# Performance work log

Measured on AMD Instinct MI355X. Metric: run time of the kernel, lower is better.

## Reference

```python
import jax, jax.numpy as jnp
import numpy as np

NUM_HEADS = 8
HEAD_DIM = 128
ATTN_SCALE = 0.12


def _rotary_tables(T, head_dim, dtype=jnp.float32):
    # modded-nanogpt half-truncated RoPE: rotate only first half of freq slots
    quarter = head_dim // 4
    angular = (1.0 / 1024.0) ** jnp.linspace(0.0, 1.0, quarter, dtype=dtype)
    angular = jnp.concatenate([angular, jnp.zeros(quarter, dtype=dtype)])  # [head_dim//2]
    t = jnp.arange(T, dtype=dtype)
    theta = t[:, None] * angular[None, :]  # [T, head_dim//2]
    return jnp.cos(theta), jnp.sin(theta)


def _apply_rotary(x, cos, sin):
    # x: [B, T, H, D]; cos/sin: [T, D//2]
    x1, x2 = jnp.split(x, 2, axis=-1)
    c = cos[None, :, None, :]
    s = sin[None, :, None, :]
    y1 = x1 * c + x2 * s
    y2 = -x1 * s + x2 * c
    return jnp.concatenate([y1, y2], axis=-1)


def _rms_norm(x):
    eps = jnp.asarray(jnp.finfo(x.dtype).eps, x.dtype)
    var = jnp.mean(jnp.square(x), axis=-1, keepdims=True)
    return x * jax.lax.rsqrt(var + eps)


def setup_inputs() -> dict:
    key = jax.random.key(0)
    k1, k2, k3, k4, k5 = jax.random.split(key, 5)
    B, T, D = 1, 4096, 1024
    hdim = NUM_HEADS * HEAD_DIM
    std = 0.5 * D ** (-0.5)
    x = jax.random.normal(k1, (B, T, D), dtype=jnp.float32)
    ve = jax.random.normal(k2, (B, T, hdim), dtype=jnp.float32)
    qkv_w = jax.random.normal(k3, (3, hdim, D), dtype=jnp.float32) * std
    lambdas = jnp.array([0.5, 0.5], dtype=jnp.float32)
    c_proj_w = jax.random.normal(k5, (D, hdim), dtype=jnp.float32) * std
    return {"x": x, "ve": ve, "qkv_w": qkv_w, "lambdas": lambdas, "c_proj_w": c_proj_w}


def reference(x, ve, qkv_w, lambdas, c_proj_w):
    B, T, D = x.shape
    H, Hd = NUM_HEADS, HEAD_DIM
    # QKV projection: qkv_w [3, H*Hd, D]
    qkv = jnp.einsum('btd,ckd->btck', x, qkv_w)  # [B, T, 3, H*Hd]
    qkv = qkv.reshape(B, T, 3, H, Hd)
    q, k, v = qkv[:, :, 0], qkv[:, :, 1], qkv[:, :, 2]  # [B, T, H, Hd]
    # QK RMSNorm
    q = _rms_norm(q)
    k = _rms_norm(k)
    # RoPE
    cos, sin = _rotary_tables(T, Hd, dtype=x.dtype)
    q = _apply_rotary(q, cos, sin)
    k = _apply_rotary(k, cos, sin)
    # value-embedding lambda mix
    v = lambdas[0] * v + lambdas[1] * ve.reshape(B, T, H, Hd)
    # causal attention with fixed scale 0.12 (block-causal FlexAttention mask)
    scores = jnp.einsum('bthd,bshd->bhts', q, k) * ATTN_SCALE  # [B, H, T, T]
    causal = jnp.tril(jnp.ones((T, T), dtype=bool))
    scores = jnp.where(causal[None, None], scores, jnp.asarray(-jnp.inf, scores.dtype))
    probs = jax.nn.softmax(scores, axis=-1)
    y = jnp.einsum('bhts,bshd->bthd', probs, v)  # [B, T, H, Hd]
    y = y.reshape(B, T, H * Hd)
    return y @ c_proj_w.T  # [B, T, D]
```

## Files before the change

### kernel.cpp

```cpp
#include <hip/hip_runtime.h>

typedef __bf16 bf16;
typedef __bf16 bf16x8 __attribute__((ext_vector_type(8)));
typedef __bf16 bf16x4 __attribute__((ext_vector_type(4)));
typedef __bf16 bf16x2 __attribute__((ext_vector_type(2)));
typedef float f32x4 __attribute__((ext_vector_type(4)));
typedef float f32x16 __attribute__((ext_vector_type(16)));
typedef int i32x4 __attribute__((ext_vector_type(4)));

#define GLL16(gp, lp)                                                          \
  __builtin_amdgcn_global_load_lds(                                            \
      (const __attribute__((address_space(1))) unsigned int*)(gp),             \
      (__attribute__((address_space(3))) unsigned int*)(lp), 16, 0, 0)

__global__ __launch_bounds__(256) void cast3_f32_bf16(
    const float* __restrict__ a, bf16* __restrict__ oa, int na4,
    const float* __restrict__ b, bf16* __restrict__ ob, int nb4,
    const float* __restrict__ c, bf16* __restrict__ oc, int nc4) {
  int i = blockIdx.x * blockDim.x + threadIdx.x;
  int stride = gridDim.x * blockDim.x;
  int total = na4 + nb4 + nc4;
  for (; i < total; i += stride) {
    const float4* src;
    bf16x4* dst;
    int j = i;
    if (j < na4) {
      src = (const float4*)a + j; dst = (bf16x4*)oa + j;
    } else if ((j -= na4) < nb4) {
      src = (const float4*)b + j; dst = (bf16x4*)ob + j;
    } else {
      j -= nb4;
      src = (const float4*)c + j; dst = (bf16x4*)oc + j;
    }
    float4 v = *src;
    bf16x4 o;
    o[0] = (bf16)v.x; o[1] = (bf16)v.y; o[2] = (bf16)v.z; o[3] = (bf16)v.w;
    *dst = o;
  }
}

template <int K, int LDC, typename CT>
__global__ __launch_bounds__(256) void gemm_bt(
    const bf16* __restrict__ A, const bf16* __restrict__ B,
    CT* __restrict__ C) {
  __shared__ __align__(16) bf16 As[128 * 64];
  __shared__ __align__(16) bf16 Bs[128 * 64];
  const int tid  = threadIdx.x;
  const int lane = tid & 63;
  const int wave = tid >> 6;
  const int ln15 = lane & 15, quad = lane >> 4;
  const int wm = wave >> 1, wn = wave & 1;
  const int m0 = blockIdx.y * 128, n0 = blockIdx.x * 128;

  f32x4 acc[4][4] = {};

  for (int k0 = 0; k0 < K; k0 += 64) {
    __syncthreads();
#pragma unroll
    for (int j = 0; j < 4; ++j) {
      int gbase = j * 256 + wave * 64;
      int g = gbase + lane;
      int r = g >> 3, c = (g & 7) ^ (r & 7);
      GLL16(A + (size_t)(m0 + r) * K + k0 + c * 8, As + (size_t)gbase * 8);
    }
#pragma unroll
    for (int j = 0; j < 4; ++j) {
      int gbase = j * 256 + wave * 64;
      int g = gbase + lane;
      int r = g >> 3, c = (g & 7) ^ (r & 7);
      GLL16(B + (size_t)(n0 + r) * K + k0 + c * 8, Bs + (size_t)gbase * 8);
    }
    __syncthreads();
#pragma unroll
    for (int kk = 0; kk < 2; ++kk) {
      bf16x8 af[4], bfr[4];
#pragma unroll
      for (int mi = 0; mi < 4; ++mi) {
        int m = wm * 64 + mi * 16 + ln15;
        int cg = kk * 4 + quad;
        af[mi] = *(const bf16x8*)(As + (m * 8 + (cg ^ (m & 7))) * 8);
      }
#pragma unroll
      for (int ni = 0; ni < 4; ++ni) {
        int n = wn * 64 + ni * 16 + ln15;
        int cg = kk * 4 + quad;
        bfr[ni] = *(const bf16x8*)(Bs + (n * 8 + (cg ^ (n & 7))) * 8);
      }
#pragma unroll
      for (int mi = 0; mi < 4; ++mi)
#pragma unroll
        for (int ni = 0; ni < 4; ++ni)
          acc[mi][ni] = __builtin_amdgcn_mfma_f32_16x16x32_bf16(
              af[mi], bfr[ni], acc[mi][ni], 0, 0, 0);
    }
  }
#pragma unroll
  for (int mi = 0; mi < 4; ++mi)
#pragma unroll
    for (int ni = 0; ni < 4; ++ni)
#pragma unroll
      for (int r = 0; r < 4; ++r) {
        int row = m0 + wm * 64 + mi * 16 + quad * 4 + r;
        int col = n0 + wn * 64 + ni * 16 + ln15;
        C[(size_t)row * LDC + col] = (CT)acc[mi][ni][r];
      }
}

__global__ __launch_bounds__(256) void qkv_post(
    const bf16* __restrict__ qkv, const float* __restrict__ ve,
    const float* __restrict__ lambdas, bf16* __restrict__ qn,
    bf16* __restrict__ kn, bf16* __restrict__ vt) {
  const int h  = blockIdx.x;
  const int t0 = blockIdx.y * 64;
  const int tid = threadIdx.x;
  const int wave = tid >> 6, lane = tid & 63;
  __shared__ __align__(16) float tile[64][129];

  const int j = lane;
  float cth = 1.0f, sth = 0.0f;
  for (int i = 0; i < 16; ++i) {
    int t = t0 + wave * 16 + i;
    if (j < 32) {
      float ang = exp2f((float)j * (-10.0f / 31.0f));
      float th = (float)t * ang;
      __sincosf(th, &sth, &cth);
    }
#pragma unroll
    for (int qk = 0; qk < 2; ++qk) {
      const bf16* row = qkv + (size_t)t * 3072 + qk * 1024 + h * 128;
      float x1 = (float)row[j], x2 = (float)row[j + 64];
      float ss = x1 * x1 + x2 * x2;
#pragma unroll
      for (int m = 1; m < 64; m <<= 1) ss += __shfl_xor(ss, m, 64);
      float rinv = rsqrtf(ss * (1.0f / 128.0f) + 1.1920929e-7f);
      if (qk == 0) rinv *= 0.12f;
      float y1 = (x1 * cth + x2 * sth) * rinv;
      float y2 = (x2 * cth - x1 * sth) * rinv;
      bf16* orow = (qk == 0 ? qn : kn) + (size_t)t * 1024 + h * 128;
      orow[j] = (bf16)y1;
      orow[j + 64] = (bf16)y2;
    }
  }

  float l0 = lambdas[0], l1 = lambdas[1];
  for (int c = 0; c < 32; ++c) {
    int idx = c * 256 + tid;
    int d = idx & 127, tl = idx >> 7;
    int t = t0 + tl;
    float v = (float)qkv[(size_t)t * 3072 + 2048 + h * 128 + d];
    float vev = ve[(size_t)t * 1024 + h * 128 + d];
    tile[tl][d] = l0 * v + l1 * vev;
  }
  __syncthreads();
  for (int c = 0; c < 32; ++c) {
    int idx = c * 256 + tid;
    int tl = idx & 63, d = idx >> 6;
    vt[((size_t)(h * 128 + d)) * 4096 + t0 + tl] = (bf16)tile[tl][d];
  }
}

__global__ __launch_bounds__(256, 2) void flash_attn(
    const bf16* __restrict__ qn, const bf16* __restrict__ kn,
    const bf16* __restrict__ vt, float* __restrict__ Op,
    float* __restrict__ ls) {
  const int id = blockIdx.x;
  const int qtile = 63 - (id >> 4);
  const int sub = id & 15;
  const int h = sub >> 1;
  const int half = sub & 1;
  const int tid = threadIdx.x;
  const int wave = tid >> 6, lane = tid & 63;
  const int l31 = lane & 31, hl = lane >> 5;
  const int qi = wave >> 1, ki = wave & 1;

  __shared__ __align__(16) bf16 smem[4 * 64 * 128];
  __shared__ float rsb[2][2][32];
  bf16* Ks = smem;
  bf16* Vs = smem + 2 * 64 * 128;

  const int q0 = qtile * 64;
  const int nkv = qtile + 1;
  const int half0 = (nkv + 1) >> 1;
  const int kt_begin = half ? half0 : 0;
  const int kt_end = half ? nkv : half0;
  const int niter = kt_end - kt_begin;
  const int pidx = (h * 64 + qtile) * 2 + half;

  if (niter == 0) {
    float4 z = {0.f, 0.f, 0.f, 0.f};
    float* opb = Op + (size_t)pidx * 8192;
#pragma unroll
    for (int j = 0; j < 8; ++j) *(float4*)(opb + tid * 32 + j * 4) = z;
    if (tid < 64) ls[pidx * 64 + tid] = 0.f;
    return;
  }

  const int qg = q0 + qi * 32 + l31;

  bf16x8 qf[8];
  {
    const bf16* qb = qn + (size_t)qg * 1024 + h * 128 + hl * 8;
#pragma unroll
    for (int f = 0; f < 8; ++f) qf[f] = *(const bf16x8*)(qb + f * 16);
  }

  f32x16 acc_o[4] = {};
  float rs = 0.0f;

  auto prefetch = [&](int kt, int buf) {
    const int kv0 = kt * 64;
    bf16* ks = Ks + buf * (64 * 128);
    bf16* vs = Vs + buf * (128 * 64);
#pragma unroll
    for (int jj = 0; jj < 4; ++jj) {
      int gbase = jj * 256 + wave * 64;
      int g = gbase + lane;
      int r = g >> 4, c = (g & 15) ^ (r & 15);
      GLL16(kn + (size_t)(kv0 + r) * 1024 + h * 128 + c * 8,
            ks + (size_t)gbase * 8);
    }
#pragma unroll
    for (int jj = 0; jj < 4; ++jj) {
      int gbase = jj * 256 + wave * 64;
      int g = gbase + lane;
      int d = g >> 3, c = (g & 7) ^ (d & 7);
      GLL16(vt + ((size_t)(h * 128 + d)) * 4096 + kv0 + c * 8,
            vs + (size_t)gbase * 8);
    }
  };

  prefetch(kt_begin, 0);

  for (int it = 0; it < niter; ++it) {
    const int kt = kt_begin + it;
    const int kv0 = kt * 64;
    __syncthreads();
    if (it + 1 < niter) prefetch(kt + 1, (it + 1) & 1);
    const bf16* ksb = Ks + (it & 1) * (64 * 128);
    const bf16* vsb = Vs + (it & 1) * (128 * 64);

    f32x16 accs = {};
    const int krow = ki * 32 + l31;
#pragma unroll
    for (int f = 0; f < 8; ++f) {
      bf16x8 a =
          *(const bf16x8*)(ksb + (krow * 16 + ((2 * f + hl) ^ (krow & 15))) * 8);
      accs = __builtin_amdgcn_mfma_f32_32x32x16_bf16(a, qf[f], accs, 0, 0, 0);
    }

    const bool diag = (kt == nkv - 1);
    float pe[16];
#pragma unroll
    for (int r = 0; r < 16; ++r) {
      int kvl = (r & 3) + 8 * (r >> 2) + 4 * hl;
      float v = __expf(accs[r]);
      if (diag && (kv0 + ki * 32 + kvl) > qg) v = 0.0f;
      rs += v;
      pe[r] = v;
    }
    int pk[8];
#pragma unroll
    for (int g = 0; g < 8; ++g) {
      bf16x2 t;
      t[0] = (bf16)pe[2 * g];
      t[1] = (bf16)pe[2 * g + 1];
      pk[g] = __builtin_bit_cast(int, t);
    }

    bf16x8 pf[2];
#pragma unroll
    for (int c = 0; c < 2; ++c) {
      int sh0 = __shfl_xor(pk[4 * c + 0], 32, 64);
      int sh1 = __shfl_xor(pk[4 * c + 1], 32, 64);
      int sh2 = __shfl_xor(pk[4 * c + 2], 32, 64);
      int sh3 = __shfl_xor(pk[4 * c + 3], 32, 64);
      int own0 = hl ? pk[4 * c + 2] : pk[4 * c + 0];
      int own1 = hl ? pk[4 * c + 3] : pk[4 * c + 1];
      int par0 = hl ? sh2 : sh0;
      int par1 = hl ? sh3 : sh1;
      i32x4 dv;
      dv[0] = hl ? par0 : own0;
      dv[1] = hl ? par1 : own1;
      dv[2] = hl ? own0 : par0;
      dv[3] = hl ? own1 : par1;
      pf[c] = __builtin_bit_cast(bf16x8, dv);
    }

#pragma unroll
    for (int dt = 0; dt < 4; ++dt) {
      int vrow = dt * 32 + l31;
#pragma unroll
      for (int c = 0; c < 2; ++c) {
        bf16x8 a = *(const bf16x8*)(
            vsb + (vrow * 8 + ((4 * ki + 2 * c + hl) ^ (vrow & 7))) * 8);
        acc_o[dt] =
            __builtin_amdgcn_mfma_f32_32x32x16_bf16(a, pf[c], acc_o[dt], 0, 0, 0);
      }
    }
  }

  rs += __shfl_xor(rs, 32, 64);
  __syncthreads();
  if (lane < 32) rsb[qi][ki][l31] = rs;
  float* ob = (float*)smem;
  if (ki == 1) {
#pragma unroll
    for (int dt = 0; dt < 4; ++dt)
#pragma unroll
      for (int r = 0; r < 16; ++r) {
        int d = dt * 32 + (r & 3) + 8 * (r >> 2) + 4 * hl;
        ob[(qi * 32 + l31) * 129 + d] = acc_o[dt][r];
      }
  }
  __syncthreads();
  if (ki == 0) {
    float lsum = rsb[qi][0][l31] + rsb[qi][1][l31];
    if (hl == 0) ls[pidx * 64 + qi * 32 + l31] = lsum;
    float* opb = Op + (size_t)pidx * 8192 + (qi * 32 + l31) * 128;
#pragma unroll
    for (int dt = 0; dt < 4; ++dt)
#pragma unroll
      for (int rg = 0; rg < 4; ++rg) {
        float4 o;
        int d0 = dt * 32 + 4 * hl + 8 * rg;
        o.x = acc_o[dt][rg * 4 + 0] + ob[(qi * 32 + l31) * 129 + d0 + 0];
        o.y = acc_o[dt][rg * 4 + 1] + ob[(qi * 32 + l31) * 129 + d0 + 1];
        o.z = acc_o[dt][rg * 4 + 2] + ob[(qi * 32 + l31) * 129 + d0 + 2];
        o.w = acc_o[dt][rg * 4 + 3] + ob[(qi * 32 + l31) * 129 + d0 + 3];
        *(float4*)(opb + d0) = o;
      }
  }
}

__global__ __launch_bounds__(256) void attn_combine(
    const float* __restrict__ Op, const float* __restrict__ ls,
    bf16* __restrict__ y) {
  int gid = blockIdx.x * 256 + threadIdx.x;
  int t = gid >> 8;
  int c4 = gid & 255;
  int qtile = t >> 6, ql = t & 63;
  int h = c4 >> 5;
  int d = (c4 & 31) * 4;
  int pbase = (h * 64 + qtile) * 2;
  const float4 o0 = *(const float4*)(Op + (size_t)pbase * 8192 + ql * 128 + d);
  const float4 o1 =
      *(const float4*)(Op + (size_t)(pbase + 1) * 8192 + ql * 128 + d);
  float inv = 1.0f / (ls[pbase * 64 + ql] + ls[(pbase + 1) * 64 + ql]);
  bf16x4 o;
  o[0] = (bf16)((o0.x + o1.x) * inv);
  o[1] = (bf16)((o0.y + o1.y) * inv);
  o[2] = (bf16)((o0.z + o1.z) * inv);
  o[3] = (bf16)((o0.w + o1.w) * inv);
  *(bf16x4*)(y + (size_t)t * 1024 + h * 128 + d) = o;
}

extern "C" void kernel_launch(void* const* d_in, const int* in_sizes, int n_in,
                              void* d_out, int out_size, void* d_ws,
                              size_t ws_size, hipStream_t stream) {
  const float* x       = (const float*)d_in[0];
  const float* ve      = (const float*)d_in[1];
  const float* qkv_w   = (const float*)d_in[2];
  const float* lambdas = (const float*)d_in[3];
  const float* c_proj  = (const float*)d_in[4];
  float* out = (float*)d_out;

  char* ws = (char*)d_ws;
  bf16* qkv   = (bf16*)ws;
  bf16* xbf   = (bf16*)(ws + 25165824);
  bf16* wqkv  = (bf16*)(ws + 33554432);
  bf16* wproj = (bf16*)(ws + 39845888);
  bf16* qn    = (bf16*)(ws + 41943040);
  bf16* kn    = (bf16*)(ws + 50331648);
  bf16* vt    = (bf16*)(ws + 58720256);
  bf16* yb    = (bf16*)(ws + 67108864);
  float* Op  = (float*)ws;
  float* lsw = (float*)(ws + 33554432);

  cast3_f32_bf16<<<2048, 256, 0, stream>>>(x, xbf, 4194304 / 4, qkv_w, wqkv,
                                           3145728 / 4, c_proj, wproj,
                                           1048576 / 4);

  gemm_bt<1024, 3072, bf16><<<dim3(24, 32), 256, 0, stream>>>(xbf, wqkv, qkv);

  qkv_post<<<dim3(8, 64), 256, 0, stream>>>(qkv, ve, lambdas, qn, kn, vt);

  flash_attn<<<1024, 256, 0, stream>>>(qn, kn, vt, Op, lsw);
  attn_combine<<<4096, 256, 0, stream>>>(Op, lsw, yb);

  gemm_bt<1024, 1024, float><<<dim3(8, 32), 256, 0, stream>>>(yb, wproj, out);
}
```

Measured before the change: 239.9 us.

## Tune attention inner loop and shrink output-projection GEMM tile

The flash attention QK^T product is split into two independent MFMA accumulator chains, MFMA sections are wrapped in s_setprio, and the causal mask check is split into a separate diagonal branch. The rest of the loop adds partial row-sum accumulators and replaces the shuffle-based P transpose with permlane32_swap where that builtin is available. The GEMM gets a BM template parameter so the output projection uses 64-row tiles, doubling its grid to 512 blocks to fill more CUs. These changes aim to cut MFMA dependency stalls and under-occupancy, at the cost of more registers and lower per-block reuse in the projection GEMM.

Result: faster. 227.1 us (-5.3%).

```diff
diff --git a/kernel.cpp b/kernel.cpp
--- a/kernel.cpp
+++ b/kernel.cpp
@@ -7,6 +7,7 @@
 typedef float f32x4 __attribute__((ext_vector_type(4)));
 typedef float f32x16 __attribute__((ext_vector_type(16)));
 typedef int i32x4 __attribute__((ext_vector_type(4)));
+typedef int i32x2 __attribute__((ext_vector_type(2)));
 
 #define GLL16(gp, lp)                                                          \
   __builtin_amdgcn_global_load_lds(                                            \
@@ -39,25 +40,26 @@
   }
 }
 
-template <int K, int LDC, typename CT>
+template <int K, int LDC, int BM, typename CT>
 __global__ __launch_bounds__(256) void gemm_bt(
     const bf16* __restrict__ A, const bf16* __restrict__ B,
     CT* __restrict__ C) {
-  __shared__ __align__(16) bf16 As[128 * 64];
+  __shared__ __align__(16) bf16 As[BM * 64];
   __shared__ __align__(16) bf16 Bs[128 * 64];
   const int tid  = threadIdx.x;
   const int lane = tid & 63;
   const int wave = tid >> 6;
   const int ln15 = lane & 15, quad = lane >> 4;
   const int wm = wave >> 1, wn = wave & 1;
-  const int m0 = blockIdx.y * 128, n0 = blockIdx.x * 128;
-
-  f32x4 acc[4][4] = {};
+  const int m0 = blockIdx.y * BM, n0 = blockIdx.x * 128;
+  constexpr int MI = BM / 32;
+
+  f32x4 acc[MI][4] = {};
 
   for (int k0 = 0; k0 < K; k0 += 64) {
     __syncthreads();
 #pragma unroll
-    for (int j = 0; j < 4; ++j) {
+    for (int j = 0; j < BM / 32; ++j) {
       int gbase = j * 256 + wave * 64;
       int g = gbase + lane;
       int r = g >> 3, c = (g & 7) ^ (r & 7);
@@ -73,10 +75,10 @@
     __syncthreads();
 #pragma unroll
     for (int kk = 0; kk < 2; ++kk) {
-      bf16x8 af[4], bfr[4];
-#pragma unroll
-      for (int mi = 0; mi < 4; ++mi) {
-        int m = wm * 64 + mi * 16 + ln15;
+      bf16x8 af[MI], bfr[4];
+#pragma unroll
+      for (int mi = 0; mi < MI; ++mi) {
+        int m = wm * (BM / 2) + mi * 16 + ln15;
         int cg = kk * 4 + quad;
         af[mi] = *(const bf16x8*)(As + (m * 8 + (cg ^ (m & 7))) * 8);
       }
@@ -87,7 +89,7 @@
         bfr[ni] = *(const bf16x8*)(Bs + (n * 8 + (cg ^ (n & 7))) * 8);
       }
 #pragma unroll
-      for (int mi = 0; mi < 4; ++mi)
+      for (int mi = 0; mi < MI; ++mi)
 #pragma unroll
         for (int ni = 0; ni < 4; ++ni)
           acc[mi][ni] = __builtin_amdgcn_mfma_f32_16x16x32_bf16(
@@ -95,12 +97,12 @@
     }
   }
 #pragma unroll
-  for (int mi = 0; mi < 4; ++mi)
+  for (int mi = 0; mi < MI; ++mi)
 #pragma unroll
     for (int ni = 0; ni < 4; ++ni)
 #pragma unroll
       for (int r = 0; r < 4; ++r) {
-        int row = m0 + wm * 64 + mi * 16 + quad * 4 + r;
+        int row = m0 + wm * (BM / 2) + mi * 16 + quad * 4 + r;
         int col = n0 + wn * 64 + ni * 16 + ln15;
         C[(size_t)row * LDC + col] = (CT)acc[mi][ni][r];
       }
@@ -239,25 +241,43 @@
     const bf16* ksb = Ks + (it & 1) * (64 * 128);
     const bf16* vsb = Vs + (it & 1) * (128 * 64);
 
-    f32x16 accs = {};
+    f32x16 acc0 = {}, acc1 = {};
     const int krow = ki * 32 + l31;
-#pragma unroll
-    for (int f = 0; f < 8; ++f) {
-      bf16x8 a =
-          *(const bf16x8*)(ksb + (krow * 16 + ((2 * f + hl) ^ (krow & 15))) * 8);
-      accs = __builtin_amdgcn_mfma_f32_32x32x16_bf16(a, qf[f], accs, 0, 0, 0);
-    }
+    __builtin_amdgcn_s_setprio(1);
+#pragma unroll
+    for (int f = 0; f < 4; ++f) {
+      bf16x8 a0 = *(const bf16x8*)(
+          ksb + (krow * 16 + ((2 * f + hl) ^ (krow & 15))) * 8);
+      bf16x8 a1 = *(const bf16x8*)(
+          ksb + (krow * 16 + ((2 * (f + 4) + hl) ^ (krow & 15))) * 8);
+      acc0 = __builtin_amdgcn_mfma_f32_32x32x16_bf16(a0, qf[f], acc0, 0, 0, 0);
+      acc1 = __builtin_amdgcn_mfma_f32_32x32x16_bf16(a1, qf[f + 4], acc1, 0, 0, 0);
+    }
+    __builtin_amdgcn_s_setprio(0);
+    f32x16 accs = acc0 + acc1;
 
     const bool diag = (kt == nkv - 1);
     float pe[16];
-#pragma unroll
-    for (int r = 0; r < 16; ++r) {
-      int kvl = (r & 3) + 8 * (r >> 2) + 4 * hl;
-      float v = __expf(accs[r]);
-      if (diag && (kv0 + ki * 32 + kvl) > qg) v = 0.0f;
-      rs += v;
-      pe[r] = v;
-    }
+    float rsp[4] = {0.f, 0.f, 0.f, 0.f};
+    if (diag) {
+#pragma unroll
+      for (int r = 0; r < 16; ++r) {
+        int kvl = (r & 3) + 8 * (r >> 2) + 4 * hl;
+        float v = __expf(accs[r]);
+        if ((kv0 + ki * 32 + kvl) > qg) v = 0.0f;
+        rsp[r & 3] += v;
+        pe[r] = v;
+      }
+    } else {
+#pragma unroll
+      for (int r = 0; r < 16; ++r) {
+        float v = __expf(accs[r]);
+        rsp[r & 3] += v;
+        pe[r] = v;
+      }
+    }
+    rs += (rsp[0] + rsp[1]) + (rsp[2] + rsp[3]);
+
     int pk[8];
 #pragma unroll
     for (int g = 0; g < 8; ++g) {
@@ -268,6 +288,21 @@
     }
 
     bf16x8 pf[2];
+#if __has_builtin(__builtin_amdgcn_permlane32_swap)
+#pragma unroll
+    for (int c = 0; c < 2; ++c) {
+      i32x2 r02 = __builtin_amdgcn_permlane32_swap(pk[4 * c + 0], pk[4 * c + 2],
+                                                   false, false);
+      i32x2 r13 = __builtin_amdgcn_permlane32_swap(pk[4 * c + 1], pk[4 * c + 3],
+                                                   false, false);
+      i32x4 dv;
+      dv[0] = r02[0];
+      dv[1] = r13[0];
+      dv[2] = r02[1];
+      dv[3] = r13[1];
+      pf[c] = __builtin_bit_cast(bf16x8, dv);
+    }
+#else
 #pragma unroll
     for (int c = 0; c < 2; ++c) {
       int sh0 = __shfl_xor(pk[4 * c + 0], 32, 64);
@@ -285,7 +320,9 @@
       dv[3] = hl ? own1 : par1;
       pf[c] = __builtin_bit_cast(bf16x8, dv);
     }
-
+#endif
+
+    __builtin_amdgcn_s_setprio(1);
 #pragma unroll
     for (int dt = 0; dt < 4; ++dt) {
       int vrow = dt * 32 + l31;
@@ -297,6 +334,7 @@
             __builtin_amdgcn_mfma_f32_32x32x16_bf16(a, pf[c], acc_o[dt], 0, 0, 0);
       }
     }
+    __builtin_amdgcn_s_setprio(0);
   }
 
   rs += __shfl_xor(rs, 32, 64);
@@ -380,12 +418,14 @@
                                            3145728 / 4, c_proj, wproj,
                                            1048576 / 4);
 
-  gemm_bt<1024, 3072, bf16><<<dim3(24, 32), 256, 0, stream>>>(xbf, wqkv, qkv);
+  gemm_bt<1024, 3072, 128, bf16><<<dim3(24, 32), 256, 0, stream>>>(xbf, wqkv,
+                                                                   qkv);
 
   qkv_post<<<dim3(8, 64), 256, 0, stream>>>(qkv, ve, lambdas, qn, kn, vt);
 
   flash_attn<<<1024, 256, 0, stream>>>(qn, kn, vt, Op, lsw);
   attn_combine<<<4096, 256, 0, stream>>>(Op, lsw, yb);
 
-  gemm_bt<1024, 1024, float><<<dim3(8, 32), 256, 0, stream>>>(yb, wproj, out);
-}
+  gemm_bt<1024, 1024, 64, float><<<dim3(8, 64), 256, 0, stream>>>(yb, wproj,
+                                                                  out);
+}
```
